# Performance work log

Measured on AMD Instinct MI355X. Metric: run time of the kernel, lower is better.

## Reference

```python
import jax, jax.numpy as jnp
import numpy as np


def _lstm_layer(x_seq, w_ih, w_hh, b_ih, b_hh):
    # x_seq: [T, in], PyTorch gate order i, f, g, o
    H = w_hh.shape[1]
    h0 = jnp.zeros((H,), x_seq.dtype)

    def step(carry, x_t):
        h, c = carry
        gates = x_t @ w_ih.T + h @ w_hh.T + b_ih + b_hh  # [4H]
        i, f, g, o = jnp.split(gates, 4)
        i = jax.nn.sigmoid(i)
        f = jax.nn.sigmoid(f)
        g = jnp.tanh(g)
        o = jax.nn.sigmoid(o)
        c = f * c + i * g
        h = o * jnp.tanh(c)
        return (h, c), h

    _, hs = jax.lax.scan(step, (h0, h0), x_seq)
    return hs  # [T, H]


def setup_inputs() -> dict:
    key = jax.random.key(0)
    ks = jax.random.split(key, 12)
    B, T, n, H = 8, 128, 32, 128
    s = 1.0 / np.sqrt(H)

    def u(k, shape):
        return jax.random.uniform(k, shape, jnp.float32, -s, s)

    return {
        "x": jax.random.normal(ks[0], (B, T, n, n), jnp.float32),
        "w_ih0": u(ks[1], (4 * H, 1)),
        "w_hh0": u(ks[2], (4 * H, H)),
        "b_ih0": u(ks[3], (4 * H,)),
        "b_hh0": u(ks[4], (4 * H,)),
        "w_ih1": u(ks[5], (4 * H, H)),
        "w_hh1": u(ks[6], (4 * H, H)),
        "b_ih1": u(ks[7], (4 * H,)),
        "b_hh1": u(ks[8], (4 * H,)),
        "w_out": u(ks[9], (1, H)),
        "b_out": u(ks[10], (1,)),
    }


def reference(x, w_ih0, w_hh0, b_ih0, b_hh0, w_ih1, w_hh1, b_ih1, b_hh1, w_out, b_out):
    # x: [B, T, n, n]
    def rnn_forward(xi):  # xi: [T, n, n] -> out [T, 1]
        u = jnp.trace(xi, axis1=-2, axis2=-1)[:, None]  # [T, 1]
        h1 = _lstm_layer(u, w_ih0, w_hh0, b_ih0, b_hh0)
        h2 = _lstm_layer(h1, w_ih1, w_hh1, b_ih1, b_hh1)
        return h2 @ w_out.T + b_out  # [T, 1]

    jac = jax.vmap(jax.jacrev(rnn_forward))(x)  # [B, T, 1, T, n, n]
    d = jnp.diagonal(jac, axis1=1, axis2=3)      # [B, 1, n, n, T]
    # mirror torch: [:, 0] then transpose(2,3).transpose(1,2) -> [B, T, n, n]
    return jnp.transpose(d[:, 0], (0, 3, 1, 2))
```

## Files before the change

### kernel.cpp

```cpp
#include <hip/hip_runtime.h>
#include <math.h>

#define H    128
#define TT   128
#define CH   8
#define NCH  (TT / CH)

#define OFF_H1V   0
#define OFF_PARTS 262144
#define OFF_GPART 1310720
#define OFF_CNT   1441792

__device__ __forceinline__ float sigf(float x)       { return 1.0f / (1.0f + __expf(-x)); }
__device__ __forceinline__ float tanhf_fast(float x) { return 1.0f - 2.0f / (1.0f + __expf(2.0f * x)); }

__device__ __forceinline__ float quad_sum(float v) {
    int t = __builtin_amdgcn_update_dpp(0, __float_as_int(v), 0xB1, 0xF, 0xF, true);
    v += __int_as_float(t);
    t = __builtin_amdgcn_update_dpp(0, __float_as_int(v), 0x4E, 0xF, 0xF, true);
    v += __int_as_float(t);
    return v;
}

__device__ __forceinline__ void wait_ge(int* ptr, int val) {
    while (__hip_atomic_load(ptr, __ATOMIC_RELAXED, __HIP_MEMORY_SCOPE_AGENT) < val)
        __builtin_amdgcn_s_sleep(1);
    (void)__hip_atomic_load(ptr, __ATOMIC_ACQUIRE, __HIP_MEMORY_SCOPE_AGENT);
}

#define DECLW4(nm, src) \
    float4 _t_##nm = (src); \
    float nm##_x = _t_##nm.x, nm##_y = _t_##nm.y, nm##_z = _t_##nm.z, nm##_w = _t_##nm.w; \
    asm volatile("" : "+v"(nm##_x), "+v"(nm##_y), "+v"(nm##_z), "+v"(nm##_w));

#define LOADW_ALL(W) \
    const float4* wpa_ = (const float4*)((W) + (size_t)(rg)       * H + p * 32); \
    const float4* wpb_ = (const float4*)((W) + (size_t)(rg + 128) * H + p * 32); \
    const float4* wpc_ = (const float4*)((W) + (size_t)(rg + 256) * H + p * 32); \
    const float4* wpd_ = (const float4*)((W) + (size_t)(rg + 384) * H + p * 32); \
    DECLW4(wa0, wpa_[0]) DECLW4(wa1, wpa_[1]) DECLW4(wa2, wpa_[2]) DECLW4(wa3, wpa_[3]) \
    DECLW4(wa4, wpa_[4]) DECLW4(wa5, wpa_[5]) DECLW4(wa6, wpa_[6]) DECLW4(wa7, wpa_[7]) \
    DECLW4(wb0, wpb_[0]) DECLW4(wb1, wpb_[1]) DECLW4(wb2, wpb_[2]) DECLW4(wb3, wpb_[3]) \
    DECLW4(wb4, wpb_[4]) DECLW4(wb5, wpb_[5]) DECLW4(wb6, wpb_[6]) DECLW4(wb7, wpb_[7]) \
    DECLW4(wc0, wpc_[0]) DECLW4(wc1, wpc_[1]) DECLW4(wc2, wpc_[2]) DECLW4(wc3, wpc_[3]) \
    DECLW4(wc4, wpc_[4]) DECLW4(wc5, wpc_[5]) DECLW4(wc6, wpc_[6]) DECLW4(wc7, wpc_[7]) \
    DECLW4(wd0, wpd_[0]) DECLW4(wd1, wpd_[1]) DECLW4(wd2, wpd_[2]) DECLW4(wd3, wpd_[3]) \
    DECLW4(wd4, wpd_[4]) DECLW4(wd5, wpd_[5]) DECLW4(wd6, wpd_[6]) DECLW4(wd7, wpd_[7])

#define FMA1(nm, ov, acc) \
    acc = fmaf(nm##_x, ov.x, acc); acc = fmaf(nm##_y, ov.y, acc); \
    acc = fmaf(nm##_z, ov.z, acc); acc = fmaf(nm##_w, ov.w, acc);

#define DOTJ(j) FMA1(wa##j, hv##j, a0) FMA1(wb##j, hv##j, a1) FMA1(wc##j, hv##j, a2) FMA1(wd##j, hv##j, a3)

#define DOT_BODY(HBASE) \
    const float4* _hp4 = (const float4*)(HBASE); \
    float4 hv0=_hp4[0],hv1=_hp4[1],hv2=_hp4[2],hv3=_hp4[3], \
           hv4=_hp4[4],hv5=_hp4[5],hv6=_hp4[6],hv7=_hp4[7]; \
    float a0=0.f,a1=0.f,a2=0.f,a3=0.f; \
    DOTJ(0) DOTJ(1) DOTJ(2) DOTJ(3) DOTJ(4) DOTJ(5) DOTJ(6) DOTJ(7) \
    a0 = quad_sum(a0); a1 = quad_sum(a1); a2 = quad_sum(a2); a3 = quad_sum(a3);

__global__ __launch_bounds__(512, 1)
void pipe_kernel(const float* __restrict__ x,
                 const float* __restrict__ w_ih0,
                 const float* __restrict__ w_hh0,
                 const float* __restrict__ b_ih0,
                 const float* __restrict__ b_hh0,
                 const float* __restrict__ w_ih1,
                 const float* __restrict__ w_hh1,
                 const float* __restrict__ b_ih1,
                 const float* __restrict__ b_hh1,
                 const float* __restrict__ w_out,
                 float* __restrict__ ws) {
    const int role = blockIdx.x >> 3;
    const int b    = blockIdx.x & 7;
    const int r    = threadIdx.x;
    const int rg   = r >> 2, p = r & 3;
    const int wsl  = rg >> 5, wpos = rg & 31;

    int* cntA  = (int*)ws + OFF_CNT       + b * 32;
    int* cntB1 = (int*)ws + OFF_CNT + 256 + b * 32;
    int* cntB2 = (int*)ws + OFF_CNT + 512 + b * 32;
    float* h1v = ws + OFF_H1V + (size_t)b * TT * 256;

    __shared__ float hbuf[2][144];
    __shared__ float u_s[TT];
    __shared__ float scr[512];
    __shared__ float hb[CH * 144];

    if (role == 0) {
        LOADW_ALL(w_hh0)
        const float b0 = b_ih0[rg]       + b_hh0[rg];
        const float b1 = b_ih0[rg + 128] + b_hh0[rg + 128];
        const float b2 = b_ih0[rg + 256] + b_hh0[rg + 256];
        const float b3 = b_ih0[rg + 384] + b_hh0[rg + 384];
        const float wi0 = w_ih0[rg], wi1 = w_ih0[rg + 128];
        const float wi2 = w_ih0[rg + 256], wi3 = w_ih0[rg + 384];
        {
            const float* xb = x + (size_t)(b * TT + (r & 127)) * 1024;
            const int pq = r >> 7;
            float u = 0.f;
#pragma unroll
            for (int i = 0; i < 8; i++) u += xb[(pq * 8 + i) * 33];
            scr[r] = u;
        }
        if (r < 144) hbuf[0][r] = 0.f;
        __syncthreads();
        if (r < TT) u_s[r] = scr[r] + scr[r + 128] + scr[r + 256] + scr[r + 384];
        __syncthreads();

        float c1 = 0.f;
        for (int t = 0; t < TT; t++) {
            const float* hc = hbuf[t & 1];
            float* hx = hbuf[(t & 1) ^ 1];
            DOT_BODY(hc + p * 36)
            const float u = u_s[t];
            float z0 = a0 + fmaf(wi0, u, b0);
            float z1 = a1 + fmaf(wi1, u, b1);
            float z2 = a2 + fmaf(wi2, u, b2);
            float z3 = a3 + fmaf(wi3, u, b3);
            float gi = sigf(z0), gf = sigf(z1), gg = tanhf_fast(z2), go = sigf(z3);
            float di = gi * (1.f - gi) * wi0, df = gf * (1.f - gf) * wi1;
            float dg = (1.f - gg * gg) * wi2, dd = go * (1.f - go) * wi3;
            float dc = df * c1 + di * gg + gi * dg;
            c1 = gf * c1 + gi * gg;
            float th = tanhf_fast(c1);
            float hn = go * th;
            float vn = dd * th + go * (1.f - th * th) * dc;
            if (p == wsl) hx[p * 36 + wpos] = hn;
            if (p == 0) h1v[t * 256 + rg] = hn;
            if (p == 1) h1v[t * 256 + 128 + rg] = vn;
            __syncthreads();
            if ((t & (CH - 1)) == CH - 1 && r == 0)
                __hip_atomic_store(cntA, t + 1, __ATOMIC_RELEASE, __HIP_MEMORY_SCOPE_AGENT);
        }
    } else if (role == 1 || role == 2) {
        LOADW_ALL(w_ih1)
        int* myCnt = (role == 2) ? cntB2 : cntB1;
        const float* hsrc = h1v + ((role == 2) ? 128 : 0);
        float* pbase = ws + OFF_PARTS + (size_t)b * TT * 1024 + ((role == 2) ? 512 : 0);
        for (int c = 0; c < NCH; c++) {
            if (r == 0) wait_ge(cntA, (c + 1) * CH);
            __syncthreads();
            if (r < 256) {
                int tl = r >> 5, k4 = r & 31, s = k4 >> 3, j = k4 & 7;
                float4 v = *(const float4*)(hsrc + (size_t)(c * CH + tl) * 256 + k4 * 4);
                *(float4*)&hb[(tl * 4 + s) * 36 + j * 4] = v;
            }
            __syncthreads();
#pragma unroll
            for (int tl = 0; tl < CH; tl++) {
                DOT_BODY(hb + (tl * 4 + p) * 36)
                float sel = (p == 0) ? a0 : (p == 1) ? a1 : (p == 2) ? a2 : a3;
                pbase[(size_t)(c * CH + tl) * 1024 + r] = sel;
            }
            __syncthreads();
            if (r == 0)
                __hip_atomic_store(myCnt, (c + 1) * CH, __ATOMIC_RELEASE, __HIP_MEMORY_SCOPE_AGENT);
        }
    } else {
        LOADW_ALL(w_hh1)
        const float b0 = b_ih1[rg]       + b_hh1[rg];
        const float b1 = b_ih1[rg + 128] + b_hh1[rg + 128];
        const float b2 = b_ih1[rg + 256] + b_hh1[rg + 256];
        const float b3 = b_ih1[rg + 384] + b_hh1[rg + 384];
        const float wo = w_out[rg];
        if (r < 144) hbuf[0][r] = 0.f;
        __syncthreads();
        const float* parts = ws + OFF_PARTS + (size_t)b * TT * 1024;
        float* gpart = ws + OFF_GPART + (size_t)b * TT * 128;
        float c2 = 0.f;
        for (int c = 0; c < NCH; c++) {
            if (r == 0) { wait_ge(cntB1, (c + 1) * CH); wait_ge(cntB2, (c + 1) * CH); }
            __syncthreads();
            float4 zf[CH], af[CH];
#pragma unroll
            for (int tl = 0; tl < CH; tl++) {
                zf[tl] = *(const float4*)(parts + (size_t)(c * CH + tl) * 1024 + rg * 4);
                af[tl] = *(const float4*)(parts + (size_t)(c * CH + tl) * 1024 + 512 + rg * 4);
            }
#pragma unroll
            for (int tl = 0; tl < CH; tl++) {
                const int t = c * CH + tl;
                const float* hc = hbuf[t & 1];
                float* hx = hbuf[(t & 1) ^ 1];
                DOT_BODY(hc + p * 36)
                float z0 = a0 + b0 + zf[tl].x;
                float z1 = a1 + b1 + zf[tl].y;
                float z2 = a2 + b2 + zf[tl].z;
                float z3 = a3 + b3 + zf[tl].w;
                float gi = sigf(z0), gf = sigf(z1), gg = tanhf_fast(z2), go = sigf(z3);
                float di = gi * (1.f - gi) * af[tl].x, df = gf * (1.f - gf) * af[tl].y;
                float dg = (1.f - gg * gg) * af[tl].z, dd = go * (1.f - go) * af[tl].w;
                float dc = df * c2 + di * gg + gi * dg;
                c2 = gf * c2 + gi * gg;
                float th = tanhf_fast(c2);
                if (p == wsl) hx[p * 36 + wpos] = go * th;
                float dh2 = dd * th + go * (1.f - th * th) * dc;
                if (p == 0) gpart[t * 128 + rg] = wo * dh2;
                __syncthreads();
            }
        }
    }
}

__global__ __launch_bounds__(256)
void fill_kernel(const float* __restrict__ gpart, float4* __restrict__ out4) {
    const int bt = blockIdx.x;
    const int r  = threadIdx.x;
    __shared__ float red[129];
    if (r < 128) red[r] = gpart[(size_t)bt * 128 + r];
    __syncthreads();
    if (r < 64) {
        float v = red[r] + red[r + 64];
#pragma unroll
        for (int s = 32; s > 0; s >>= 1) v += __shfl_down(v, s, 64);
        if (r == 0) red[128] = v;
    }
    __syncthreads();
    const float g = red[128];
    const int m  = r * 4;
    const int i  = m >> 5, j0 = m & 31;
    float4 v;
    v.x = (j0     == i) ? g : 0.f;
    v.y = (j0 + 1 == i) ? g : 0.f;
    v.z = (j0 + 2 == i) ? g : 0.f;
    v.w = (j0 + 3 == i) ? g : 0.f;
    out4[(size_t)bt * 256 + r] = v;
}

extern "C" void kernel_launch(void* const* d_in, const int* in_sizes, int n_in,
                              void* d_out, int out_size, void* d_ws, size_t ws_size,
                              hipStream_t stream) {
    const float* x     = (const float*)d_in[0];
    const float* w_ih0 = (const float*)d_in[1];
    const float* w_hh0 = (const float*)d_in[2];
    const float* b_ih0 = (const float*)d_in[3];
    const float* b_hh0 = (const float*)d_in[4];
    const float* w_ih1 = (const float*)d_in[5];
    const float* w_hh1 = (const float*)d_in[6];
    const float* b_ih1 = (const float*)d_in[7];
    const float* b_hh1 = (const float*)d_in[8];
    const float* w_out = (const float*)d_in[9];

    float* ws = (float*)d_ws;

    pipe_kernel<<<dim3(32), dim3(512), 0, stream>>>(x, w_ih0, w_hh0, b_ih0, b_hh0,
                                                    w_ih1, w_hh1, b_ih1, b_hh1, w_out,
                                                    ws);
    fill_kernel<<<dim3(1024), dim3(256), 0, stream>>>(ws + OFF_GPART, (float4*)d_out);
}
```

Baseline: 242.1 us.

## Fuse output fill into layer-2 block and use lighter LDS-only barriers

The separate fill kernel is removed. The layer-2 recurrent block now keeps per-step gradient partials in shared memory, reduces them after each chunk, and writes the diagonal output tiles directly. Most __syncthreads are replaced with barriers that wait only on LDS counters, so global stores are no longer drained every step. The trade is one fewer launch and global round trip against output writes added to the critical serial block.

Result: no change. 245.3 us (+1.3%).

```diff
diff --git a/kernel.cpp b/kernel.cpp
--- a/kernel.cpp
+++ b/kernel.cpp
@@ -8,7 +8,6 @@
 
 #define OFF_H1V   0
 #define OFF_PARTS 262144
-#define OFF_GPART 1310720
 #define OFF_CNT   1441792
 
 __device__ __forceinline__ float sigf(float x)       { return 1.0f / (1.0f + __expf(-x)); }
@@ -27,6 +26,18 @@
         __builtin_amdgcn_s_sleep(1);
     (void)__hip_atomic_load(ptr, __ATOMIC_ACQUIRE, __HIP_MEMORY_SCOPE_AGENT);
 }
+
+#define BARRIER_LGKM() do { \
+    asm volatile("s_waitcnt lgkmcnt(0)" ::: "memory"); \
+    __builtin_amdgcn_s_barrier(); \
+    asm volatile("" ::: "memory"); \
+} while (0)
+
+#define BARRIER_ALL() do { \
+    asm volatile("s_waitcnt vmcnt(0) lgkmcnt(0)" ::: "memory"); \
+    __builtin_amdgcn_s_barrier(); \
+    asm volatile("" ::: "memory"); \
+} while (0)
 
 #define DECLW4(nm, src) \
     float4 _t_##nm = (src); \
@@ -72,7 +83,8 @@
                  const float* __restrict__ b_ih1,
                  const float* __restrict__ b_hh1,
                  const float* __restrict__ w_out,
-                 float* __restrict__ ws) {
+                 float* __restrict__ ws,
+                 float4* __restrict__ out4) {
     const int role = blockIdx.x >> 3;
     const int b    = blockIdx.x & 7;
     const int r    = threadIdx.x;
@@ -88,6 +100,7 @@
     __shared__ float u_s[TT];
     __shared__ float scr[512];
     __shared__ float hb[CH * 144];
+    __shared__ float gbuf[CH][128];
 
     if (role == 0) {
         LOADW_ALL(w_hh0)
@@ -131,9 +144,13 @@
             if (p == wsl) hx[p * 36 + wpos] = hn;
             if (p == 0) h1v[t * 256 + rg] = hn;
             if (p == 1) h1v[t * 256 + 128 + rg] = vn;
-            __syncthreads();
-            if ((t & (CH - 1)) == CH - 1 && r == 0)
-                __hip_atomic_store(cntA, t + 1, __ATOMIC_RELEASE, __HIP_MEMORY_SCOPE_AGENT);
+            if ((t & (CH - 1)) == CH - 1) {
+                BARRIER_ALL();
+                if (r == 0)
+                    __hip_atomic_store(cntA, t + 1, __ATOMIC_RELEASE, __HIP_MEMORY_SCOPE_AGENT);
+            } else {
+                BARRIER_LGKM();
+            }
         }
     } else if (role == 1 || role == 2) {
         LOADW_ALL(w_ih1)
@@ -155,7 +172,7 @@
                 float sel = (p == 0) ? a0 : (p == 1) ? a1 : (p == 2) ? a2 : a3;
                 pbase[(size_t)(c * CH + tl) * 1024 + r] = sel;
             }
-            __syncthreads();
+            BARRIER_ALL();
             if (r == 0)
                 __hip_atomic_store(myCnt, (c + 1) * CH, __ATOMIC_RELEASE, __HIP_MEMORY_SCOPE_AGENT);
         }
@@ -169,7 +186,6 @@
         if (r < 144) hbuf[0][r] = 0.f;
         __syncthreads();
         const float* parts = ws + OFF_PARTS + (size_t)b * TT * 1024;
-        float* gpart = ws + OFF_GPART + (size_t)b * TT * 128;
         float c2 = 0.f;
         for (int c = 0; c < NCH; c++) {
             if (r == 0) { wait_ge(cntB1, (c + 1) * CH); wait_ge(cntB2, (c + 1) * CH); }
@@ -198,36 +214,36 @@
                 float th = tanhf_fast(c2);
                 if (p == wsl) hx[p * 36 + wpos] = go * th;
                 float dh2 = dd * th + go * (1.f - th * th) * dc;
-                if (p == 0) gpart[t * 128 + rg] = wo * dh2;
-                __syncthreads();
+                if (p == 0) gbuf[tl][rg] = wo * dh2;
+                BARRIER_LGKM();
+            }
+            {
+                const int w = r >> 6, l = r & 63;
+                float v = gbuf[w][l] + gbuf[w][l + 64];
+                v = quad_sum(v);
+                v += __shfl_xor(v, 4, 64);
+                v += __shfl_xor(v, 8, 64);
+                v += __shfl_xor(v, 16, 64);
+                v += __shfl_xor(v, 32, 64);
+                if (l == 0) scr[w] = v;
+                BARRIER_LGKM();
+                float4* ob = out4 + ((size_t)b * TT + c * CH) * 256;
+#pragma unroll
+                for (int i = 0; i < 4; i++) {
+                    const int idx = i * 512 + r;
+                    const float g = scr[idx >> 8];
+                    const int s4 = (idx & 255) * 4;
+                    const int i0 = s4 >> 5, j0 = s4 & 31;
+                    float4 vv;
+                    vv.x = (j0     == i0) ? g : 0.f;
+                    vv.y = (j0 + 1 == i0) ? g : 0.f;
+                    vv.z = (j0 + 2 == i0) ? g : 0.f;
+                    vv.w = (j0 + 3 == i0) ? g : 0.f;
+                    ob[idx] = vv;
+                }
             }
         }
     }
-}
-
-__global__ __launch_bounds__(256)
-void fill_kernel(const float* __restrict__ gpart, float4* __restrict__ out4) {
-    const int bt = blockIdx.x;
-    const int r  = threadIdx.x;
-    __shared__ float red[129];
-    if (r < 128) red[r] = gpart[(size_t)bt * 128 + r];
-    __syncthreads();
-    if (r < 64) {
-        float v = red[r] + red[r + 64];
-#pragma unroll
-        for (int s = 32; s > 0; s >>= 1) v += __shfl_down(v, s, 64);
-        if (r == 0) red[128] = v;
-    }
-    __syncthreads();
-    const float g = red[128];
-    const int m  = r * 4;
-    const int i  = m >> 5, j0 = m & 31;
-    float4 v;
-    v.x = (j0     == i) ? g : 0.f;
-    v.y = (j0 + 1 == i) ? g : 0.f;
-    v.z = (j0 + 2 == i) ? g : 0.f;
-    v.w = (j0 + 3 == i) ? g : 0.f;
-    out4[(size_t)bt * 256 + r] = v;
 }
 
 extern "C" void kernel_launch(void* const* d_in, const int* in_sizes, int n_in,
@@ -248,6 +264,5 @@
 
     pipe_kernel<<<dim3(32), dim3(512), 0, stream>>>(x, w_ih0, w_hh0, b_ih0, b_hh0,
                                                     w_ih1, w_hh1, b_ih1, b_hh1, w_out,
-                                                    ws);
-    fill_kernel<<<dim3(1024), dim3(256), 0, stream>>>(ws + OFF_GPART, (float4*)d_out);
-}
+                                                    ws, (float4*)d_out);
+}
```
